# Optimization experiments

Measured on AMD Instinct MI355X. Metric: run time of the kernel, lower is better.

Reference implementation:

```python
import jax, jax.numpy as jnp
import numpy as np

H, C = 5, 64            # attention heads, per-head channels (out_channels=conv_dim)
NEG_SLOPE = 0.2         # GATv2 leaky_relu slope
N_NODES = 50000

def setup_inputs() -> dict:
    key = jax.random.key(0)
    ks = jax.random.split(key, 10)
    N, E = N_NODES, 400000
    node_dim, edge_dim = 128, 16
    s = 0.1
    return {
        'x': jax.random.normal(ks[0], (N, node_dim), jnp.float32),
        'edge_index': jax.random.randint(ks[1], (2, E), 0, N),
        'edge_attr': jax.random.normal(ks[2], (E, edge_dim), jnp.float32),
        'W0': jax.random.normal(ks[3], (node_dim, H * C), jnp.float32) * s,
        'b0': jnp.zeros((H * C,), jnp.float32),
        'We0': jax.random.normal(ks[4], (edge_dim, H * C), jnp.float32) * s,
        'att0': jax.random.normal(ks[5], (H, C), jnp.float32) * s,
        'bias0': jnp.zeros((C,), jnp.float32),
        'W12': jax.random.normal(ks[6], (2, C, H * C), jnp.float32) * s,
        'b12': jnp.zeros((2, H * C), jnp.float32),
        'We12': jax.random.normal(ks[7], (2, edge_dim, H * C), jnp.float32) * s,
        'att12': jax.random.normal(ks[8], (2, H, C), jnp.float32) * s,
        'bias12': jnp.zeros((2, C), jnp.float32),
    }

def _add_self_loops_mean(edge_index, edge_attr, N):
    # PyG add_self_loops(fill_value='mean'): self-loop attr = mean of incoming edge attrs per dst node
    dst = edge_index[1]
    sums = jax.ops.segment_sum(edge_attr, dst, num_segments=N)
    cnt = jax.ops.segment_sum(jnp.ones((edge_attr.shape[0], 1), edge_attr.dtype), dst, num_segments=N)
    loop_attr = sums / jnp.maximum(cnt, 1.0)
    loop = jnp.arange(N, dtype=edge_index.dtype)
    ei = jnp.concatenate([edge_index, jnp.stack([loop, loop])], axis=1)
    ea = jnp.concatenate([edge_attr, loop_attr], axis=0)
    return ei, ea

def _gatv2_layer(x, src, dst, eattr, W, b, We, att, bias, N):
    h = (x @ W + b).reshape(N, H, C)                     # shared lin_l==lin_r (share_weights=True)
    e = (eattr @ We).reshape(-1, H, C)                   # lin_edge (no bias)
    s = jax.nn.leaky_relu(h[src] + h[dst] + e, NEG_SLOPE)  # [E', H, C]
    logits = jnp.einsum('ehc,hc->eh', s, att)            # [E', H]
    m = jax.ops.segment_max(logits, dst, num_segments=N)
    m = jnp.where(jnp.isfinite(m), m, 0.0)
    ex = jnp.exp(logits - m[dst])
    denom = jax.ops.segment_sum(ex, dst, num_segments=N) + 1e-16
    alpha = ex / denom[dst]                              # per-dst softmax (dropout off: eval mode)
    msg = h[src] * alpha[:, :, None]
    out = jax.ops.segment_sum(msg, dst, num_segments=N)  # [N, H, C]
    return out.mean(axis=1) + bias                       # concat=False -> head mean, then bias

def reference(x, edge_index, edge_attr, W0, b0, We0, att0, bias0, W12, b12, We12, att12, bias12):
    N = x.shape[0]
    ei, ea = _add_self_loops_mean(edge_index, edge_attr, N)
    src, dst = ei[0], ei[1]
    h = jax.nn.elu(_gatv2_layer(x, src, dst, ea, W0, b0, We0, att0, bias0, N))
    for i in range(2):
        h = jax.nn.elu(_gatv2_layer(h, src, dst, ea, W12[i], b12[i], We12[i], att12[i], bias12[i], N))
    return h  # jk_mode='last'
```

## Files before the change

kernel.cpp:

```cpp
#include <hip/hip_runtime.h>
#include <hip/hip_fp16.h>
#include <math.h>

#define NH 5
#define NC 64
#define ED 16
#define HC 320
#define CH 32

typedef _Float16 h2  __attribute__((ext_vector_type(2)));
typedef _Float16 v8h __attribute__((ext_vector_type(8)));
typedef float    v4f __attribute__((ext_vector_type(4)));

template<int ctrl, int rmask>
__device__ __forceinline__ float dpp_add(float x) {
    int y = __builtin_amdgcn_update_dpp(0, __float_as_int(x), ctrl, rmask, 0xf, true);
    return x + __int_as_float(y);
}
__device__ __forceinline__ float wave_sum_all(float x) {
    x = dpp_add<0xb1, 0xf>(x);
    x = dpp_add<0x4e, 0xf>(x);
    x = dpp_add<0x114, 0xf>(x);
    x = dpp_add<0x118, 0xf>(x);
    x = dpp_add<0x142, 0xa>(x);
    x = dpp_add<0x143, 0xc>(x);
    return __int_as_float(__builtin_amdgcn_readlane(__float_as_int(x), 63));
}


__global__ void count_kernel(const int* __restrict__ dst, int* __restrict__ cnt, int E) {
    int t = blockIdx.x * blockDim.x + threadIdx.x;
    if (t >= E) return;
    atomicAdd(&cnt[dst[t]], 1);
}

__global__ void scan_kernel(const int* __restrict__ cnt, int* __restrict__ offsets,
                            int* __restrict__ cursor, int N) {
    __shared__ int sums[1024];
    int t = threadIdx.x;
    int chunk = (N + 1023) / 1024;
    int beg = t * chunk;
    int end = min(beg + chunk, N);
    int s = 0;
    for (int i = beg; i < end; ++i) s += cnt[i] + 1;
    sums[t] = s;
    __syncthreads();
    for (int o = 1; o < 1024; o <<= 1) {
        int v = (t >= o) ? sums[t - o] : 0;
        __syncthreads();
        sums[t] += v;
        __syncthreads();
    }
    int run = (t > 0) ? sums[t - 1] : 0;
    for (int i = beg; i < end; ++i) {
        offsets[i] = run; cursor[i] = run;
        run += cnt[i] + 1;
    }
    if (t == 0) offsets[N] = sums[1023];
}

__global__ void scatter_kernel(const int* __restrict__ src, const int* __restrict__ dst,
                               int* __restrict__ cursor, int2* __restrict__ recs, int N, int E) {
    int t = blockIdx.x * blockDim.x + threadIdx.x;
    if (t >= E + N) return;
    int d, s;
    if (t < E) { d = dst[t]; s = src[t]; }
    else       { d = t - E; s = t - E; }
    int pos = atomicAdd(&cursor[d], 1);
    recs[pos] = make_int2(s, t);
}

__global__ void loop_from_csr(const int* __restrict__ offsets, const int2* __restrict__ recs,
                              const float* __restrict__ ea, float* __restrict__ loop,
                              int N, int E) {
    int t = blockIdx.x * blockDim.x + threadIdx.x;
    int n = t >> 4, k = t & 15;
    if (n >= N) return;
    int beg = offsets[n], end = offsets[n + 1];
    float s = 0.f; int c = 0;
    for (int j = beg; j < end; ++j) {
        int y = recs[j].y;
        if (y < E) { s += ea[(size_t)y * ED + k]; ++c; }
    }
    loop[(size_t)n * ED + k] = s / (float)max(c, 1);
}

__global__ void reorder_ea(const int2* __restrict__ recs, const float* __restrict__ ea,
                           const float* __restrict__ loop, h2* __restrict__ easrt,
                           int R, int E) {
    int t = blockIdx.x * blockDim.x + threadIdx.x;
    int slot = t >> 3, k2 = t & 7;
    if (slot >= R) return;
    int y = recs[slot].y;
    const float2* sp = (const float2*)((y < E) ? ea + (size_t)y * ED : loop + (size_t)(y - E) * ED);
    float2 f = sp[k2];
    h2 o; o.x = (_Float16)f.x; o.y = (_Float16)f.y;
    easrt[(size_t)slot * 8 + k2] = o;
}

__global__ void win_start_kernel(const int* __restrict__ offsets, int* __restrict__ winStart, int N) {
    int i = blockIdx.x * blockDim.x + threadIdx.x;
    if (i >= N) return;
    atomicMin(&winStart[offsets[i] / CH], i);
}

__global__ void cvt_f16(const float* __restrict__ in, _Float16* __restrict__ out, int n) {
    int i = blockIdx.x * blockDim.x + threadIdx.x;
    if (i < n) out[i] = (_Float16)in[i];
}

__global__ void transpose_w(const float* __restrict__ W, _Float16* __restrict__ Wt, int K) {
    int t = blockIdx.x * blockDim.x + threadIdx.x;
    if (t >= 320 * K) return;
    int k = t / 320, n = t % 320;
    Wt[(size_t)n * K + k] = (_Float16)W[t];
}

__global__ __launch_bounds__(256) void gemm_mfma(const _Float16* __restrict__ A,
                                                 const _Float16* __restrict__ Bt,
                                                 const float* __restrict__ bias,
                                                 _Float16* __restrict__ Cout, int M, int K) {
    int lane = threadIdx.x & 63;
    int wave = threadIdx.x >> 6;
    int m = lane & 15, quad = lane >> 4;
    int rowBase = (blockIdx.x * 4 + wave) * 16;
    if (rowBase >= M) return;

    v4f acc[20];
#pragma unroll
    for (int c = 0; c < 20; ++c) acc[c] = (v4f){0.f, 0.f, 0.f, 0.f};

    for (int k0 = 0; k0 < K; k0 += 32) {
        v8h a = *(const v8h*)&A[(size_t)(rowBase + m) * K + k0 + quad * 8];
#pragma unroll
        for (int c = 0; c < 20; ++c) {
            v8h b = *(const v8h*)&Bt[(size_t)(c * 16 + m) * K + k0 + quad * 8];
            acc[c] = __builtin_amdgcn_mfma_f32_16x16x32_f16(a, b, acc[c], 0, 0, 0);
        }
    }
#pragma unroll
    for (int c = 0; c < 20; ++c) {
        float bb = bias[c * 16 + m];
#pragma unroll
        for (int r = 0; r < 4; ++r) {
            int row = rowBase + quad * 4 + r;
            Cout[(size_t)row * HC + c * 16 + m] = (_Float16)(acc[c][r] + bb);
        }
    }
}

__global__ __launch_bounds__(256) void gat_fused(const _Float16* __restrict__ hbuf,
                                                 const int* __restrict__ offsets,
                                                 const int2* __restrict__ recs,
                                                 const h2* __restrict__ easrt,
                                                 const int* __restrict__ winStart,
                                                 const float* __restrict__ We,
                                                 const float* __restrict__ att,
                                                 const float* __restrict__ bias,
                                                 _Float16* __restrict__ outH,
                                                 float* __restrict__ outF,
                                                 int N, int R) {
    int lane = threadIdx.x & 63;
    int wave = (blockIdx.x * blockDim.x + threadIdx.x) >> 6;
    int totalWaves = (gridDim.x * blockDim.x) >> 6;

    h2 we2[8 * NH];
#pragma unroll
    for (int k2 = 0; k2 < 8; ++k2)
#pragma unroll
        for (int h = 0; h < NH; ++h) {
            h2 w;
            w.x = (_Float16)We[(2 * k2) * HC + h * NC + lane];
            w.y = (_Float16)We[(2 * k2 + 1) * HC + h * NC + lane];
            we2[k2 * NH + h] = w;
        }
    float attc6[NH], attc4[NH];
#pragma unroll
    for (int h = 0; h < NH; ++h) {
        float a = att[h * NC + lane];
        attc6[h] = 0.6f * a;
        attc4[h] = 0.4f * a;
    }
    float bc = bias[lane];

    for (int w = wave; w * CH < R; w += totalWaves) {
        int i = winStart[w];
        if (i >= N) continue;
        int winEnd = w * CH + CH;
        for (; i < N; ++i) {
            int beg = offsets[i];
            if (beg >= winEnd) break;
            int end = offsets[i + 1];

            const _Float16* dp = hbuf + (size_t)i * HC + lane;
            float hd[NH];
#pragma unroll
            for (int h = 0; h < NH; ++h) hd[h] = (float)dp[h * NC];

            float l[NH] = {}, acc[NH] = {};
            for (int t = beg; t < end; ++t) {
                int src = recs[t].x;
                const h2* ap = easrt + (size_t)t * 8;
                h2 a[8];
#pragma unroll
                for (int k2 = 0; k2 < 8; ++k2) a[k2] = ap[k2];
                const _Float16* sp = hbuf + (size_t)src * HC + lane;
                float hs[NH];
#pragma unroll
                for (int h = 0; h < NH; ++h) hs[h] = (float)sp[h * NC];

                float p[NH];
#pragma unroll
                for (int h = 0; h < NH; ++h) {
                    float v = hs[h] + hd[h];
#pragma unroll
                    for (int k2 = 0; k2 < 8; ++k2)
                        v = __builtin_amdgcn_fdot2(a[k2], we2[k2 * NH + h], v, false);
                    p[h] = fmaf(fabsf(v), attc4[h], v * attc6[h]);
                }
#pragma unroll
                for (int h = 0; h < NH; ++h) {
                    float pe = __expf(wave_sum_all(p[h]));
                    l[h] += pe;
                    acc[h] = fmaf(pe, hs[h], acc[h]);
                }
            }
            float o = 0.f;
#pragma unroll
            for (int h = 0; h < NH; ++h) o += acc[h] / l[h];
            o = o * 0.2f + bc;
            o = o > 0.f ? o : expm1f(o);
            if (outF) outF[(size_t)i * NC + lane] = o;
            else      outH[(size_t)i * NC + lane] = (_Float16)o;
        }
    }
}

extern "C" void kernel_launch(void* const* d_in, const int* in_sizes, int n_in,
                              void* d_out, int out_size, void* d_ws, size_t ws_size,
                              hipStream_t stream) {
    const float* x     = (const float*)d_in[0];
    const int*   ei    = (const int*)d_in[1];
    const float* ea    = (const float*)d_in[2];
    const float* W0    = (const float*)d_in[3];
    const float* b0    = (const float*)d_in[4];
    const float* We0   = (const float*)d_in[5];
    const float* att0  = (const float*)d_in[6];
    const float* bias0 = (const float*)d_in[7];
    const float* W12   = (const float*)d_in[8];
    const float* b12   = (const float*)d_in[9];
    const float* We12  = (const float*)d_in[10];
    const float* att12 = (const float*)d_in[11];
    const float* bias12= (const float*)d_in[12];

    int N = in_sizes[0] / 128;
    int E = in_sizes[1] / 2;
    int R = E + N;
    int numWin = (R + CH - 1) / CH;
    const int* srcArr = ei;
    const int* dstArr = ei + E;

    char* ws = (char*)d_ws;
    size_t off = 0;
    auto alloc = [&](size_t bytes) -> void* {
        void* p = ws + off;
        off = (off + bytes + 255) & ~(size_t)255;
        return p;
    };
    int*      cnt     = (int*)alloc((size_t)N * 4);
    int*      offsets = (int*)alloc((size_t)(N + 1) * 4);
    int*      cursor  = (int*)alloc((size_t)N * 4);
    int2*     recs    = (int2*)alloc((size_t)R * 8);
    float*    loop    = (float*)alloc((size_t)N * ED * 4);
    _Float16* hbuf    = (_Float16*)alloc((size_t)N * HC * 2);
    _Float16* acth    = (_Float16*)alloc((size_t)N * NC * 2);
    _Float16* xh      = (_Float16*)alloc((size_t)N * 128 * 2);
    _Float16* Wth0    = (_Float16*)alloc((size_t)320 * 128 * 2);
    _Float16* Wth1    = (_Float16*)alloc((size_t)320 * 64 * 2);
    _Float16* Wth2    = (_Float16*)alloc((size_t)320 * 64 * 2);
    int*      winStart= (int*)alloc((size_t)(numWin + 1) * 4);
    h2*       easrt   = (h2*)alloc((size_t)R * 32);

    (void)hipMemsetAsync(cnt, 0, (size_t)N * 4, stream);
    (void)hipMemsetAsync(winStart, 0x7f, (size_t)(numWin + 1) * 4, stream);
    count_kernel<<<(E + 255) / 256, 256, 0, stream>>>(dstArr, cnt, E);
    scan_kernel<<<1, 1024, 0, stream>>>(cnt, offsets, cursor, N);
    scatter_kernel<<<(E + N + 255) / 256, 256, 0, stream>>>(srcArr, dstArr, cursor, recs, N, E);
    loop_from_csr<<<((size_t)N * ED + 255) / 256, 256, 0, stream>>>(offsets, recs, ea, loop, N, E);
    reorder_ea<<<((size_t)R * 8 + 255) / 256, 256, 0, stream>>>(recs, ea, loop, easrt, R, E);
    win_start_kernel<<<(N + 255) / 256, 256, 0, stream>>>(offsets, winStart, N);
    cvt_f16<<<((size_t)N * 128 + 255) / 256, 256, 0, stream>>>(x, xh, N * 128);
    transpose_w<<<(320 * 128 + 255) / 256, 256, 0, stream>>>(W0, Wth0, 128);
    transpose_w<<<(320 * 64 + 255) / 256, 256, 0, stream>>>(W12, Wth1, 64);
    transpose_w<<<(320 * 64 + 255) / 256, 256, 0, stream>>>(W12 + 64 * HC, Wth2, 64);

    float* dout = (float*)d_out;
    int gemmBlocks = (N / 16 + 3) / 4 + 1;
    int fusedBlocks = 2048;

    const _Float16* As[3]  = {xh, acth, acth};
    const _Float16* Bts[3] = {Wth0, Wth1, Wth2};
    int Ks[3] = {128, 64, 64};
    const float* bs[3]   = {b0, b12, b12 + HC};
    const float* Wes[3]  = {We0, We12, We12 + ED * HC};
    const float* atts[3] = {att0, att12, att12 + NH * NC};
    const float* bis[3]  = {bias0, bias12, bias12 + NC};
    for (int layer = 0; layer < 3; ++layer) {
        gemm_mfma<<<gemmBlocks, 256, 0, stream>>>(As[layer], Bts[layer], bs[layer], hbuf, N, Ks[layer]);
        gat_fused<<<fusedBlocks, 256, 0, stream>>>(hbuf, offsets, recs, easrt, winStart,
                                                   Wes[layer], atts[layer], bis[layer],
                                                   acth, (layer == 2) ? dout : nullptr, N, R);
    }
}
```

Before: 871.0 us.

## Store node features channel-major with padded heads for vector gathers

The GEMM epilogue goes through LDS and writes h in a [node][channel][head padded to 8] layout. Each lane in the GAT kernel can then fetch all five heads of its channel with a single 16-byte load, where before it issued five scattered 2-byte loads, for both the source gather and the destination row. The log2(e) factor is folded into the attention weights so exp2f replaces __expf, and the edge index is made wave-uniform with readfirstlane. In exchange the hbuf footprint grows by 8/5 because of the padding, and the GEMM gains LDS staging and block barriers.

```diff
diff --git a/kernel.cpp b/kernel.cpp
--- a/kernel.cpp
+++ b/kernel.cpp
@@ -6,6 +6,7 @@
 #define NC 64
 #define ED 16
 #define HC 320
+#define HP 8
 #define CH 32
 
 typedef _Float16 h2  __attribute__((ext_vector_type(2)));
@@ -120,32 +121,49 @@
                                                  const _Float16* __restrict__ Bt,
                                                  const float* __restrict__ bias,
                                                  _Float16* __restrict__ Cout, int M, int K) {
+    __shared__ _Float16 lds[4][8][NC * HP];
     int lane = threadIdx.x & 63;
     int wave = threadIdx.x >> 6;
     int m = lane & 15, quad = lane >> 4;
     int rowBase = (blockIdx.x * 4 + wave) * 16;
-    if (rowBase >= M) return;
+    bool active = rowBase < M;
 
     v4f acc[20];
 #pragma unroll
     for (int c = 0; c < 20; ++c) acc[c] = (v4f){0.f, 0.f, 0.f, 0.f};
 
-    for (int k0 = 0; k0 < K; k0 += 32) {
-        v8h a = *(const v8h*)&A[(size_t)(rowBase + m) * K + k0 + quad * 8];
-#pragma unroll
-        for (int c = 0; c < 20; ++c) {
-            v8h b = *(const v8h*)&Bt[(size_t)(c * 16 + m) * K + k0 + quad * 8];
-            acc[c] = __builtin_amdgcn_mfma_f32_16x16x32_f16(a, b, acc[c], 0, 0, 0);
-        }
-    }
-#pragma unroll
-    for (int c = 0; c < 20; ++c) {
-        float bb = bias[c * 16 + m];
-#pragma unroll
-        for (int r = 0; r < 4; ++r) {
-            int row = rowBase + quad * 4 + r;
-            Cout[(size_t)row * HC + c * 16 + m] = (_Float16)(acc[c][r] + bb);
-        }
+    if (active) {
+        for (int k0 = 0; k0 < K; k0 += 32) {
+            v8h a = *(const v8h*)&A[(size_t)(rowBase + m) * K + k0 + quad * 8];
+#pragma unroll
+            for (int c = 0; c < 20; ++c) {
+                v8h b = *(const v8h*)&Bt[(size_t)(c * 16 + m) * K + k0 + quad * 8];
+                acc[c] = __builtin_amdgcn_mfma_f32_16x16x32_f16(a, b, acc[c], 0, 0, 0);
+            }
+        }
+    }
+#pragma unroll
+    for (int pass = 0; pass < 2; ++pass) {
+        if (active && (quad >> 1) == pass) {
+#pragma unroll
+            for (int c = 0; c < 20; ++c) {
+                int cc = c * 16 + m;
+                int idx = (cc & 63) * HP + (cc >> 6);
+                float bb = bias[cc];
+#pragma unroll
+                for (int r = 0; r < 4; ++r)
+                    lds[wave][(quad & 1) * 4 + r][idx] = (_Float16)(acc[c][r] + bb);
+            }
+        }
+        __syncthreads();
+        if (active) {
+#pragma unroll
+            for (int rr = 0; rr < 8; ++rr) {
+                v8h v = *(const v8h*)&lds[wave][rr][lane * HP];
+                *(v8h*)&Cout[(size_t)(rowBase + pass * 8 + rr) * (NC * HP) + lane * HP] = v;
+            }
+        }
+        __syncthreads();
     }
 }
 
@@ -174,12 +192,13 @@
             w.y = (_Float16)We[(2 * k2 + 1) * HC + h * NC + lane];
             we2[k2 * NH + h] = w;
         }
+    const float L2E = 1.4426950408889634f;
     float attc6[NH], attc4[NH];
 #pragma unroll
     for (int h = 0; h < NH; ++h) {
         float a = att[h * NC + lane];
-        attc6[h] = 0.6f * a;
-        attc4[h] = 0.4f * a;
+        attc6[h] = 0.6f * a * L2E;
+        attc4[h] = 0.4f * a * L2E;
     }
     float bc = bias[lane];
 
@@ -192,22 +211,23 @@
             if (beg >= winEnd) break;
             int end = offsets[i + 1];
 
-            const _Float16* dp = hbuf + (size_t)i * HC + lane;
+            v8h hdv = *(const v8h*)&hbuf[(size_t)i * (NC * HP) + lane * HP];
             float hd[NH];
 #pragma unroll
-            for (int h = 0; h < NH; ++h) hd[h] = (float)dp[h * NC];
+            for (int h = 0; h < NH; ++h) hd[h] = (float)hdv[h];
 
             float l[NH] = {}, acc[NH] = {};
             for (int t = beg; t < end; ++t) {
-                int src = recs[t].x;
-                const h2* ap = easrt + (size_t)t * 8;
+                int tu = __builtin_amdgcn_readfirstlane(t);
+                int src = recs[tu].x;
+                const h2* ap = easrt + (size_t)tu * 8;
                 h2 a[8];
 #pragma unroll
                 for (int k2 = 0; k2 < 8; ++k2) a[k2] = ap[k2];
-                const _Float16* sp = hbuf + (size_t)src * HC + lane;
+                v8h hsv = *(const v8h*)&hbuf[(size_t)src * (NC * HP) + lane * HP];
                 float hs[NH];
 #pragma unroll
-                for (int h = 0; h < NH; ++h) hs[h] = (float)sp[h * NC];
+                for (int h = 0; h < NH; ++h) hs[h] = (float)hsv[h];
 
                 float p[NH];
 #pragma unroll
@@ -220,7 +240,7 @@
                 }
 #pragma unroll
                 for (int h = 0; h < NH; ++h) {
-                    float pe = __expf(wave_sum_all(p[h]));
+                    float pe = exp2f(wave_sum_all(p[h]));
                     l[h] += pe;
                     acc[h] = fmaf(pe, hs[h], acc[h]);
                 }
@@ -272,7 +292,7 @@
     int*      cursor  = (int*)alloc((size_t)N * 4);
     int2*     recs    = (int2*)alloc((size_t)R * 8);
     float*    loop    = (float*)alloc((size_t)N * ED * 4);
-    _Float16* hbuf    = (_Float16*)alloc((size_t)N * HC * 2);
+    _Float16* hbuf    = (_Float16*)alloc((size_t)N * NC * HP * 2);
     _Float16* acth    = (_Float16*)alloc((size_t)N * NC * 2);
     _Float16* xh      = (_Float16*)alloc((size_t)N * 128 * 2);
     _Float16* Wth0    = (_Float16*)alloc((size_t)320 * 128 * 2);
```

Result: no change. 876.2 us (+0.6%).
